# Kernel tuning notes

Measured on AMD Instinct MI355X. Metric: run time of the kernel, lower is better.

Reference implementation:

```python
import jax, jax.numpy as jnp
import numpy as np

B = 65536        # batch of class observations
NUM_CLASSES = 100
D = 128          # embedding_latent_dim / MLP width
H = 64           # rnn_hidden_dim == vq_embedding_dim (must match when use_vq)
K = 512          # vq_num_embeddings
S = 16           # num_splines
A = 6            # spline_action_dim
SQUISH = 0.2
BETA = 0.25      # vq commitment cost


def setup_inputs() -> dict:
    key = jax.random.key(0)
    ks = jax.random.split(key, 32)
    g = lambda i, shape, s=0.05: jax.random.normal(ks[i], shape, jnp.float32) * s
    return dict(
        obs=jax.random.randint(ks[0], (B,), 0, NUM_CLASSES, dtype=jnp.int32),
        embed=g(1, (NUM_CLASSES, D)),
        W1=g(2, (D, D)), b1=jnp.zeros((D,), jnp.float32),
        W2=g(3, (D, D)), b2=jnp.zeros((D,), jnp.float32),
        W3=g(4, (D, D)), b3=jnp.zeros((D,), jnp.float32),
        Wc=g(5, (D, H)), bc=jnp.zeros((H,), jnp.float32),      # carry_init
        Wi=g(6, (D, H)), bi=jnp.zeros((H,), jnp.float32),      # SimpleCell input dense
        Wh=g(7, (H, H)),                                       # SimpleCell recurrent (no bias)
        vq_emb=g(8, (K, H)),                                   # VQ codebook
        Wm=g(9, (H, A)), bm=jnp.zeros((A,), jnp.float32),      # actor mean head
        Ws=g(10, (H, A)), bs=jnp.zeros((A,), jnp.float32),     # actor scale head
        Vw1=g(11, (D, D)), vb1=jnp.zeros((D,), jnp.float32),
        Vw2=g(12, (D, D)), vb2=jnp.zeros((D,), jnp.float32),
        Vw3=g(13, (D, 32)), vb3=jnp.zeros((32,), jnp.float32),
        Vw4=g(14, (32, 1)), vb4=jnp.zeros((1,), jnp.float32),
    )


def reference(obs, embed, W1, b1, W2, b2, W3, b3, Wc, bc, Wi, bi, Wh, vq_emb,
              Wm, bm, Ws, bs, Vw1, vb1, Vw2, vb2, Vw3, vb3, Vw4, vb4):
    # class embedding + ReLU MLP trunk
    z = embed[obs]                                # (B, D)
    z = jax.nn.relu(z @ W1 + b1)
    z = jax.nn.relu(z @ W2 + b2)
    z = jax.nn.relu(z @ W3 + b3)

    carry0 = z @ Wc + bc                          # (B, H) initial RNN carry
    emb_sq = jnp.sum(vq_emb ** 2, axis=1)         # (K,) precomputed codebook norms

    def step(carry, _):
        # SimpleCell: h = tanh(Dense(inputs) + Dense_h(carry)); inputs = z each step
        h = jnp.tanh(z @ Wi + bi + carry @ Wh)    # (B, H)
        # VQ nearest-neighbor lookup
        d = jnp.sum(h ** 2, axis=1, keepdims=True) - 2.0 * (h @ vq_emb.T) + emb_sq  # (B, K)
        idx = jnp.argmin(d, axis=1)               # (B,)
        quant = jnp.take(vq_emb, idx, axis=0)     # (B, H) == one_hot(idx) @ vq_emb
        q = h + jax.lax.stop_gradient(quant - h)  # straight-through estimator
        e_loss = jnp.mean((jax.lax.stop_gradient(q) - h) ** 2)
        q_loss = jnp.mean((q - jax.lax.stop_gradient(h)) ** 2)
        vq_loss_i = q_loss + BETA * e_loss
        # spline heads (use_tanh_last=False -> sigmoid, temp=1)
        am = jax.nn.sigmoid(q @ Wm + bm)                    # (B, A)
        sd = jax.nn.sigmoid(q @ Ws + bs) * SQUISH + 1e-8    # (B, A)
        return q, (am, sd, vq_loss_i, idx)

    _, (ams, sds, losses, idxs) = jax.lax.scan(step, carry0, None, length=S)
    # (S, B, A) -> (B, S*A), matching concatenate along axis 1 in step order
    actor_mean = jnp.transpose(ams, (1, 0, 2)).reshape(B, S * A)
    actor_scale_diag = jnp.transpose(sds, (1, 0, 2)).reshape(B, S * A)

    # critic MLP (tanh activations)
    c = jnp.tanh(z @ Vw1 + vb1)
    c = jnp.tanh(c @ Vw2 + vb2)
    c = jnp.tanh(c @ Vw3 + vb3)
    critic = jnp.squeeze(c @ Vw4 + vb4, axis=-1)  # (B,)

    total_vq_loss = jnp.sum(losses)
    return actor_mean, actor_scale_diag, critic, total_vq_loss, idxs
```

## Files before the change

kernel.cpp:

```cpp
#include <hip/hip_runtime.h>
#include <cmath>


#define D_ 128
#define H_ 64
#define K_ 512
#define S_ 16
#define B_ 65536
#define NTBL_ 64
#define NH_ 16

#define OAM   ((size_t)0)
#define OSD   ((size_t)(B_ * 96))
#define OCRIT ((size_t)(2 * B_ * 96))
#define OLOSS ((size_t)(2 * B_ * 96 + B_))
#define OIDX  ((size_t)(2 * B_ * 96 + B_ + 1))

#define WS_VQWH   0
#define WS_AM8    (512 * 64)
#define WS_SD8    (WS_AM8 + 512 * 8)
#define WS_EMBSQ  (WS_SD8 + 512 * 8)
#define WS_CNTP   (WS_EMBSQ + 512)
#define WS_CLIDX  (WS_CNTP + 2048)
#define WS_CLAM   (WS_CLIDX + 128 * 16)
#define WS_CLSD   (WS_CLAM + 128 * 96)
#define WS_CLCR   (WS_CLSD + 128 * 96)
#define WS_CLLOSS (WS_CLCR + 128)

__device__ int g_tflag = 0;

typedef const __attribute__((address_space(1))) void GASV;
typedef __attribute__((address_space(3))) void LASV;
__device__ __forceinline__ void gll16(const void* g, void* l)
{
    __builtin_amdgcn_global_load_lds((GASV*)g, (LASV*)l, 16, 0, 0);
}

template <int N4>
__device__ __forceinline__ void dma_lin(float4* __restrict__ dst,
                                        const float4* __restrict__ src,
                                        int wid, int lane)
{
    constexpr int PER = N4 / 8;
#pragma unroll
    for (int j = 0; j < PER; j += 64) {
        const int f = wid * PER + j;
        gll16(src + f + lane, dst + f);
    }
}

__global__ __launch_bounds__(512)
__attribute__((amdgpu_waves_per_eu(2, 2)))
void class_kernel(
    const int* __restrict__ obs, int* __restrict__ cnt_part, int nclass,
    const float* __restrict__ embed,
    const float* __restrict__ W1, const float* __restrict__ b1,
    const float* __restrict__ W2, const float* __restrict__ b2,
    const float* __restrict__ W3, const float* __restrict__ b3,
    const float* __restrict__ Wc, const float* __restrict__ bc,
    const float* __restrict__ Wi, const float* __restrict__ bi,
    const float* __restrict__ Wh,
    const float* __restrict__ Wm, const float* __restrict__ bm,
    const float* __restrict__ Wsw, const float* __restrict__ bs,
    const float* __restrict__ Vw1, const float* __restrict__ vb1,
    const float* __restrict__ Vw2, const float* __restrict__ vb2,
    const float* __restrict__ Vw3, const float* __restrict__ vb3,
    const float* __restrict__ Vw4, const float* __restrict__ vb4,
    float* __restrict__ vqwh, float* __restrict__ am8,
    float* __restrict__ sd8, float* __restrict__ embsq,
    const float* __restrict__ vq_emb,
    float* __restrict__ clam, float* __restrict__ clsd,
    float* __restrict__ clcr, float* __restrict__ clidx,
    float* __restrict__ clloss)
{
    extern __shared__ float4 dyn4[];
    float* __restrict__ Af    = reinterpret_cast<float*>(dyn4);
    float* __restrict__ Bf    = reinterpret_cast<float*>(dyn4 + 4096);
    float* __restrict__ vqwhL = reinterpret_cast<float*>(dyn4);
    __shared__ float zA[128], zB[128];
    __shared__ float psum[512];
    __shared__ float t1s[64], c0s[64], c3s[32];
    __shared__ float vw4s[32] __attribute__((aligned(16)));
    __shared__ float Wh_s[64 * 64] __attribute__((aligned(16)));
    __shared__ float hcand[2][4][64] __attribute__((aligned(16)));
    __shared__ float rD2[2][4];
    __shared__ int   rK2[2][4];
    __shared__ int   gk_s[16];
    __shared__ float gd_s[16];
    __shared__ float hh_s[16];

    const int bx   = blockIdx.x;
    const int tid  = threadIdx.x;
    const int lane = tid & 63;
    const int wid  = tid >> 6;

    if (bx < NTBL_) {
        float* __restrict__ er = reinterpret_cast<float*>(dyn4) + wid * 64;
        const int k = bx * 8 + wid;
        er[lane] = vq_emb[k * 64 + lane];
        __syncthreads();

        float acc = 0.f;
#pragma unroll 8
        for (int dd = 0; dd < 64; ++dd)
            acc = fmaf(er[dd], Wh[dd * 64 + lane], acc);
        vqwh[k * 64 + lane] = acc;

        float sq = er[lane] * er[lane];
#pragma unroll
        for (int m = 1; m < 64; m <<= 1) sq += __shfl_xor(sq, m);
        if (lane == 0) embsq[k] = sq;

        if (lane < 8) {
            float vm = 0.f, vs = 0.f;
            if (lane < 6) {
                vm = bm[lane];
                vs = bs[lane];
                for (int dd = 0; dd < 64; ++dd) {
                    vm = fmaf(er[dd], Wm[dd * 6 + lane], vm);
                    vs = fmaf(er[dd], Wsw[dd * 6 + lane], vs);
                }
                vm = 1.f / (1.f + expf(-vm));
                vs = 1.f / (1.f + expf(-vs)) * 0.2f + 1e-8f;
            }
            am8[k * 8 + lane] = vm;
            sd8[k * 8 + lane] = vs;
        }
        __syncthreads();
        if (tid == 0) {
            __threadfence();
            __hip_atomic_fetch_add(&g_tflag, 1, __ATOMIC_RELEASE,
                                   __HIP_MEMORY_SCOPE_AGENT);
        }
        return;
    }

    if (bx < NTBL_ + NH_) {
        int* __restrict__ hsh = reinterpret_cast<int*>(psum);
        if (tid < 128) hsh[tid] = 0;
        __syncthreads();
        const int hb = bx - NTBL_;
        for (int i = hb * 512 + tid; i < B_; i += NH_ * 512)
            atomicAdd(&hsh[obs[i]], 1);
        __syncthreads();
        if (tid < 128) cnt_part[hb * 128 + tid] = hsh[tid];
        return;
    }

    const int c = bx - NTBL_ - NH_;
    const float4* __restrict__ vq4   = reinterpret_cast<const float4*>(vq_emb);
    const float4* __restrict__ vqwh4 = reinterpret_cast<const float4*>(vqwh);

    const int j128 = tid & 127;
    const int q4   = tid >> 7;

    dma_lin<4096>(dyn4, reinterpret_cast<const float4*>(W1), wid, lane);
    if (tid < 128) zA[tid] = embed[c * 128 + tid];
    __syncthreads();

#define DENSE128(SRCW, ZSRC, ZDST, BIAS, ACT)                                  \
    {                                                                          \
        float a0 = 0.f, a1 = 0.f, a2 = 0.f, a3 = 0.f;                          \
        const int i0 = q4 * 32;                                                \
        _Pragma("unroll 8")                                                    \
        for (int ii = 0; ii < 32; ii += 4) {                                   \
            a0 = fmaf(ZSRC[i0 + ii + 0], SRCW[(i0 + ii + 0) * 128 + j128], a0);\
            a1 = fmaf(ZSRC[i0 + ii + 1], SRCW[(i0 + ii + 1) * 128 + j128], a1);\
            a2 = fmaf(ZSRC[i0 + ii + 2], SRCW[(i0 + ii + 2) * 128 + j128], a2);\
            a3 = fmaf(ZSRC[i0 + ii + 3], SRCW[(i0 + ii + 3) * 128 + j128], a3);\
        }                                                                      \
        psum[q4 * 128 + j128] = (a0 + a1) + (a2 + a3);                         \
    }                                                                          \
    __syncthreads();                                                           \
    if (tid < 128) {                                                           \
        float v = BIAS[tid] + ((psum[tid] + psum[128 + tid]) +                 \
                               (psum[256 + tid] + psum[384 + tid]));           \
        ZDST[tid] = ACT;                                                       \
    }                                                                          \
    __syncthreads();

    dma_lin<4096>(dyn4 + 4096, reinterpret_cast<const float4*>(W2), wid, lane);
    DENSE128(Af, zA, zB, b1, fmaxf(v, 0.f))

    dma_lin<4096>(dyn4, reinterpret_cast<const float4*>(W3), wid, lane);
    DENSE128(Bf, zB, zA, b2, fmaxf(v, 0.f))

    dma_lin<2048>(dyn4 + 4096, reinterpret_cast<const float4*>(Wi), wid, lane);
    dma_lin<2048>(dyn4 + 6144, reinterpret_cast<const float4*>(Wc), wid, lane);
    DENSE128(Af, zA, zB, b3, fmaxf(v, 0.f))

    if (tid == 0) {
        while (__hip_atomic_load(&g_tflag, __ATOMIC_RELAXED,
                                 __HIP_MEMORY_SCOPE_AGENT) < NTBL_)
            __builtin_amdgcn_s_sleep(2);
        __builtin_amdgcn_fence(__ATOMIC_ACQUIRE, "agent");
    }
    __syncthreads();

    dma_lin<4096>(dyn4, vqwh4, wid, lane);
    dma_lin<1024>(reinterpret_cast<float4*>(Wh_s),
                  reinterpret_cast<const float4*>(Wh), wid, lane);
    {
        const int jj = tid & 63;
        const int qq = (tid >> 6) & 3;
        const bool isC = tid >= 256;
        const float* __restrict__ Wsrc = isC ? (Bf + 8192) : Bf;
        float a0 = 0.f, a1 = 0.f, a2 = 0.f, a3 = 0.f;
        const int i0 = qq * 32;
#pragma unroll 8
        for (int ii = 0; ii < 32; ii += 4) {
            a0 = fmaf(zB[i0 + ii + 0], Wsrc[(i0 + ii + 0) * 64 + jj], a0);
            a1 = fmaf(zB[i0 + ii + 1], Wsrc[(i0 + ii + 1) * 64 + jj], a1);
            a2 = fmaf(zB[i0 + ii + 2], Wsrc[(i0 + ii + 2) * 64 + jj], a2);
            a3 = fmaf(zB[i0 + ii + 3], Wsrc[(i0 + ii + 3) * 64 + jj], a3);
        }
        psum[(isC ? 256 : 0) + qq * 64 + jj] = (a0 + a1) + (a2 + a3);
    }
    __syncthreads();

    dma_lin<4096>(dyn4 + 4096, vqwh4 + 4096, wid, lane);
    if (tid < 64) {
        t1s[tid] = bi[tid] + ((psum[tid] + psum[64 + tid]) +
                              (psum[128 + tid] + psum[192 + tid]));
    } else if (tid < 128) {
        const int j = tid - 64;
        c0s[j] = bc[j] + ((psum[256 + j] + psum[320 + j]) +
                          (psum[384 + j] + psum[448 + j]));
    } else if (tid < 160) {
        vw4s[tid - 128] = Vw4[tid - 128];
    }
    __syncthreads();

    {
        const int j = lane;
        const int q = wid;
        float a0 = 0.f, a1 = 0.f;
        const int i0 = q * 8;
#pragma unroll
        for (int ii = 0; ii < 8; ii += 2) {
            a0 = fmaf(c0s[i0 + ii + 0], Wh_s[(i0 + ii + 0) * 64 + j], a0);
            a1 = fmaf(c0s[i0 + ii + 1], Wh_s[(i0 + ii + 1) * 64 + j], a1);
        }
        psum[q * 64 + j] = a0 + a1;
    }
    float4 cb[16], cb2[16];
    float esq = 0.f, esq2 = 0.f;
    if (wid < 4) {
        const float4* __restrict__ r1 = vq4 + (size_t)tid * 16;
        const float4* __restrict__ r2 = vq4 + (size_t)(tid + 256) * 16;
#pragma unroll
        for (int d4 = 0; d4 < 16; ++d4) { cb[d4] = r1[d4]; cb2[d4] = r2[d4]; }
#pragma unroll
        for (int d4 = 0; d4 < 16; ++d4) {
            asm volatile("" : "+v"(cb[d4].x), "+v"(cb[d4].y),
                              "+v"(cb[d4].z), "+v"(cb[d4].w));
            asm volatile("" : "+v"(cb2[d4].x), "+v"(cb2[d4].y),
                              "+v"(cb2[d4].z), "+v"(cb2[d4].w));
        }
        esq  = embsq[tid];
        esq2 = embsq[tid + 256];
    }
    __syncthreads();

    if (tid < 64) {
        float a = 0.f;
#pragma unroll
        for (int q = 0; q < 8; ++q) a += psum[q * 64 + tid];
        hcand[0][0][tid] = tanhf(a + t1s[tid]);
    }
    const float t1r = t1s[lane];
    __syncthreads();

    if (wid == 0) {
        const float h0v = hcand[0][0][lane];
        float hh = h0v * h0v;
#pragma unroll
        for (int m = 1; m < 64; m <<= 1) hh += __shfl_xor(hh, m);
        if (lane == 0) hh_s[0] = hh;
    }

    int prevw = 0;
    float ca0 = 0.f, ca1 = 0.f, ca2 = 0.f, ca3 = 0.f;
#pragma unroll 1
    for (int t = 0; t < S_; ++t) {
        const int buf = t & 1;
        if (wid < 4) {
            const float* __restrict__ cur = hcand[buf][prevw];
            float a0 = 0.f, a1 = 0.f, a2 = 0.f, a3 = 0.f;
            float b0 = 0.f, b1_ = 0.f, b2_ = 0.f, b3_ = 0.f;
#pragma unroll
            for (int d4 = 0; d4 < 16; d4 += 4) {
                const float4 h0v = *reinterpret_cast<const float4*>(cur + 4 * d4);
                a0 = fmaf(h0v.x, cb[d4].x, a0); a0 = fmaf(h0v.y, cb[d4].y, a0);
                a0 = fmaf(h0v.z, cb[d4].z, a0); a0 = fmaf(h0v.w, cb[d4].w, a0);
                b0 = fmaf(h0v.x, cb2[d4].x, b0); b0 = fmaf(h0v.y, cb2[d4].y, b0);
                b0 = fmaf(h0v.z, cb2[d4].z, b0); b0 = fmaf(h0v.w, cb2[d4].w, b0);
                const float4 h1v = *reinterpret_cast<const float4*>(cur + 4 * d4 + 4);
                a1 = fmaf(h1v.x, cb[d4 + 1].x, a1); a1 = fmaf(h1v.y, cb[d4 + 1].y, a1);
                a1 = fmaf(h1v.z, cb[d4 + 1].z, a1); a1 = fmaf(h1v.w, cb[d4 + 1].w, a1);
                b1_ = fmaf(h1v.x, cb2[d4 + 1].x, b1_); b1_ = fmaf(h1v.y, cb2[d4 + 1].y, b1_);
                b1_ = fmaf(h1v.z, cb2[d4 + 1].z, b1_); b1_ = fmaf(h1v.w, cb2[d4 + 1].w, b1_);
                const float4 h2v = *reinterpret_cast<const float4*>(cur + 4 * d4 + 8);
                a2 = fmaf(h2v.x, cb[d4 + 2].x, a2); a2 = fmaf(h2v.y, cb[d4 + 2].y, a2);
                a2 = fmaf(h2v.z, cb[d4 + 2].z, a2); a2 = fmaf(h2v.w, cb[d4 + 2].w, a2);
                b2_ = fmaf(h2v.x, cb2[d4 + 2].x, b2_); b2_ = fmaf(h2v.y, cb2[d4 + 2].y, b2_);
                b2_ = fmaf(h2v.z, cb2[d4 + 2].z, b2_); b2_ = fmaf(h2v.w, cb2[d4 + 2].w, b2_);
                const float4 h3v = *reinterpret_cast<const float4*>(cur + 4 * d4 + 12);
                a3 = fmaf(h3v.x, cb[d4 + 3].x, a3); a3 = fmaf(h3v.y, cb[d4 + 3].y, a3);
                a3 = fmaf(h3v.z, cb[d4 + 3].z, a3); a3 = fmaf(h3v.w, cb[d4 + 3].w, a3);
                b3_ = fmaf(h3v.x, cb2[d4 + 3].x, b3_); b3_ = fmaf(h3v.y, cb2[d4 + 3].y, b3_);
                b3_ = fmaf(h3v.z, cb2[d4 + 3].z, b3_); b3_ = fmaf(h3v.w, cb2[d4 + 3].w, b3_);
            }
            const float d1 = fmaf(-2.f, (a0 + a1) + (a2 + a3), esq);
            const float d2 = fmaf(-2.f, (b0 + b1_) + (b2_ + b3_), esq2);
            float bD = d1;
            int   bK = tid;
            if (d2 < bD) { bD = d2; bK = tid + 256; }
#pragma unroll
            for (int m = 1; m < 64; m <<= 1) {
                const float od = __shfl_xor(bD, m);
                const int   ok = __shfl_xor(bK, m);
                if (od < bD || (od == bD && ok < bK)) { bD = od; bK = ok; }
            }
            const float vw = vqwhL[(bK << 6) + lane];
            hcand[buf ^ 1][wid][lane] = tanhf(t1r + vw);
            if (lane == 0) { rD2[buf][wid] = bD; rK2[buf][wid] = bK; }
        } else {
            const int u = tid - 256;
            const int j = u & 127;
            const int hf = u >> 7;
            if (t == 0 || t == 1 || t == 3 || t == 4) {
                const float* __restrict__ W = (t <= 1) ? Vw1 : Vw2;
                const float* __restrict__ zsrc = (t <= 1) ? zB : zA;
                const int i0 = 64 * hf + ((t == 1 || t == 4) ? 32 : 0);
                if (t == 0 || t == 3) { ca0 = ca1 = ca2 = ca3 = 0.f; }
#pragma unroll 8
                for (int ii = 0; ii < 32; ii += 4) {
                    ca0 = fmaf(zsrc[i0 + ii + 0], W[(i0 + ii + 0) * 128 + j], ca0);
                    ca1 = fmaf(zsrc[i0 + ii + 1], W[(i0 + ii + 1) * 128 + j], ca1);
                    ca2 = fmaf(zsrc[i0 + ii + 2], W[(i0 + ii + 2) * 128 + j], ca2);
                    ca3 = fmaf(zsrc[i0 + ii + 3], W[(i0 + ii + 3) * 128 + j], ca3);
                }
                if (t == 1 || t == 4) psum[u] = (ca0 + ca1) + (ca2 + ca3);
            } else if (t == 2) {
                if (u < 128) zA[u] = tanhf(vb1[u] + psum[u] + psum[128 + u]);
            } else if (t == 5) {
                if (u < 128) zA[u] = tanhf(vb2[u] + psum[u] + psum[128 + u]);
            } else if (t == 6) {
                const int j2 = u & 31;
                const int o  = u >> 5;
                float x0 = 0.f, x1 = 0.f;
                const int i0 = 16 * o;
#pragma unroll
                for (int ii = 0; ii < 16; ii += 2) {
                    x0 = fmaf(zA[i0 + ii + 0], Vw3[(i0 + ii + 0) * 32 + j2], x0);
                    x1 = fmaf(zA[i0 + ii + 1], Vw3[(i0 + ii + 1) * 32 + j2], x1);
                }
                psum[u] = x0 + x1;
            } else if (t == 7) {
                if (u < 32) {
                    float v = vb3[u];
#pragma unroll
                    for (int o = 0; o < 8; ++o) v += psum[o * 32 + u];
                    c3s[u] = tanhf(v);
                }
            } else if (t == 8) {
                if (u == 0) {
                    float sm = vb4[0];
#pragma unroll
                    for (int i = 0; i < 32; ++i) sm = fmaf(c3s[i], vw4s[i], sm);
                    clcr[c] = sm;
                }
            }
        }
        __syncthreads();

        float gD = rD2[buf][0];
        int   gK = rK2[buf][0], winw = 0;
#pragma unroll
        for (int w = 1; w < 4; ++w)
            if (rD2[buf][w] < gD || (rD2[buf][w] == gD && rK2[buf][w] < gK)) {
                gD = rD2[buf][w]; gK = rK2[buf][w]; winw = w;
            }
        if (tid == 0) { gk_s[t] = gK; gd_s[t] = gD; }
        prevw = winw;
    }
    __syncthreads();

    for (int tt = wid + 1; tt < S_; tt += 8) {
        const int g = gk_s[tt - 1];
        const float hv = tanhf(t1r + vqwhL[(g << 6) + lane]);
        float hh = hv * hv;
#pragma unroll
        for (int m = 1; m < 64; m <<= 1) hh += __shfl_xor(hh, m);
        if (lane == 0) hh_s[tt] = hh;
    }
    __syncthreads();
    if (tid == 0) {
        float s = 0.f;
#pragma unroll
        for (int t = 0; t < S_; ++t) s += gd_s[t] + hh_s[t];
        clloss[c] = s;
    }

    if (tid < 96) {
        const int t = tid / 6;
        const int j = tid - t * 6;
        const int gk = gk_s[t];
        clam[c * 96 + tid] = am8[gk * 8 + j];
        clsd[c * 96 + tid] = sd8[gk * 8 + j];
    } else if (tid >= 96 && tid < 112) {
        const int t = tid - 96;
        clidx[c * 16 + t] = (float)gk_s[t];
    }
}

__global__ __launch_bounds__(256) void scatter_kernel(
    const int* __restrict__ obs, const float* __restrict__ clam,
    const float* __restrict__ clsd, const float* __restrict__ clcr,
    const float* __restrict__ clidx, const int* __restrict__ cnt_part,
    const float* __restrict__ clloss, int nclass, float* __restrict__ out)
{
    __shared__ int icc_s[128];
    if (blockIdx.x == 0) {
        if (threadIdx.x == 0)
            __hip_atomic_store(&g_tflag, 0, __ATOMIC_RELAXED,
                               __HIP_MEMORY_SCOPE_AGENT);
        if (threadIdx.x < 128) {
            int cc = 0;
#pragma unroll
            for (int p = 0; p < NH_; ++p)
                cc += cnt_part[p * 128 + threadIdx.x];
            icc_s[threadIdx.x] = cc;
        }
        __syncthreads();
        if (threadIdx.x == 0) {
            float s = 0.f;
            for (int c = 0; c < nclass; ++c)
                s += (float)icc_s[c] * clloss[c];
            out[OLOSS] = s * 1.25f / (65536.f * 64.f);
        }
    }

    const int n_am4 = B_ * 24;
    const int n_cr4 = B_ / 4;
    const int n_idx = B_ * 16;
    const int tot   = 2 * n_am4 + n_cr4 + n_idx;
    float4* __restrict__ out4 = reinterpret_cast<float4*>(out);

    for (int i = blockIdx.x * 256 + threadIdx.x; i < tot; i += gridDim.x * 256) {
        if (i < 2 * n_am4) {
            const bool in_am = (i < n_am4);
            const int  i4    = in_am ? i : i - n_am4;
            const uint32_t row =
                (uint32_t)(((uint64_t)(i4 >> 3) * 0xAAAAAAABull) >> 33);
            const int col4 = i4 - (int)row * 24;
            const int cc   = obs[row];
            const float* __restrict__ tab = in_am ? clam : clsd;
            out4[i] = *reinterpret_cast<const float4*>(tab + cc * 96 + col4 * 4);
        } else if (i < 2 * n_am4 + n_cr4) {
            const int j = i - 2 * n_am4;
            const int r = 4 * j;
            float4 v;
            v.x = clcr[obs[r + 0]];
            v.y = clcr[obs[r + 1]];
            v.z = clcr[obs[r + 2]];
            v.w = clcr[obs[r + 3]];
            out4[i] = v;
        } else {
            const int j = i - (2 * n_am4 + n_cr4);
            const int t = j >> 16;
            const int r = j & (B_ - 1);
            out[OIDX + (size_t)j] = clidx[obs[r] * 16 + t];
        }
    }
}

extern "C" void kernel_launch(void* const* d_in, const int* in_sizes, int n_in,
                              void* d_out, int out_size, void* d_ws, size_t ws_size,
                              hipStream_t stream)
{
    const int*   obs   = (const int*)  d_in[0];
    const float* embed = (const float*)d_in[1];
    const float* W1    = (const float*)d_in[2];
    const float* b1    = (const float*)d_in[3];
    const float* W2    = (const float*)d_in[4];
    const float* b2    = (const float*)d_in[5];
    const float* W3    = (const float*)d_in[6];
    const float* b3    = (const float*)d_in[7];
    const float* Wc    = (const float*)d_in[8];
    const float* bc    = (const float*)d_in[9];
    const float* Wi    = (const float*)d_in[10];
    const float* bi    = (const float*)d_in[11];
    const float* Wh    = (const float*)d_in[12];
    const float* vq    = (const float*)d_in[13];
    const float* Wm    = (const float*)d_in[14];
    const float* bm    = (const float*)d_in[15];
    const float* Ws    = (const float*)d_in[16];
    const float* bs    = (const float*)d_in[17];
    const float* Vw1   = (const float*)d_in[18];
    const float* vb1   = (const float*)d_in[19];
    const float* Vw2   = (const float*)d_in[20];
    const float* vb2   = (const float*)d_in[21];
    const float* Vw3   = (const float*)d_in[22];
    const float* vb3   = (const float*)d_in[23];
    const float* Vw4   = (const float*)d_in[24];
    const float* vb4   = (const float*)d_in[25];

    const int nclass = in_sizes[1] / D_;

    float* ws_f     = (float*)d_ws;
    float* vqwh     = ws_f + WS_VQWH;
    float* am8      = ws_f + WS_AM8;
    float* sd8      = ws_f + WS_SD8;
    float* embsq    = ws_f + WS_EMBSQ;
    int*   cnt_part = (int*)(ws_f + WS_CNTP);
    float* clidx    = ws_f + WS_CLIDX;
    float* clam     = ws_f + WS_CLAM;
    float* clsd     = ws_f + WS_CLSD;
    float* clcr     = ws_f + WS_CLCR;
    float* clloss   = ws_f + WS_CLLOSS;

    float* out = (float*)d_out;

    class_kernel<<<NTBL_ + NH_ + nclass, 512, 131072, stream>>>(
        obs, cnt_part, nclass,
        embed, W1, b1, W2, b2, W3, b3, Wc, bc, Wi, bi, Wh,
        Wm, bm, Ws, bs,
        Vw1, vb1, Vw2, vb2, Vw3, vb3, Vw4, vb4,
        vqwh, am8, sd8, embsq, vq,
        clam, clsd, clcr, clidx, clloss);
    scatter_kernel<<<2048, 256, 0, stream>>>(obs, clam, clsd, clcr, clidx,
                                             cnt_part, clloss, nclass, out);
}
```

Before: 59.34 us.

## Move critic MLP layers out of the VQ loop and overlap them with carry setup

The critic's first two dense layers no longer run in pieces inside the first recurrent steps. They now run on the upper four waves at the same time as the lower waves compute the fused carry/input projection and the recurrent product, using a separate partial-sum buffer. The codebook-derived tables move from the workspace to __device__ globals, a few loops are unrolled further, and the acquire fence after the spin-wait on the table flag is removed. That dropped fence risks a memory-ordering bug, and the lower waves now do two recurrent partial products each.

```diff
diff --git a/kernel.cpp b/kernel.cpp
--- a/kernel.cpp
+++ b/kernel.cpp
@@ -16,18 +16,18 @@
 #define OLOSS ((size_t)(2 * B_ * 96 + B_))
 #define OIDX  ((size_t)(2 * B_ * 96 + B_ + 1))
 
-#define WS_VQWH   0
-#define WS_AM8    (512 * 64)
-#define WS_SD8    (WS_AM8 + 512 * 8)
-#define WS_EMBSQ  (WS_SD8 + 512 * 8)
-#define WS_CNTP   (WS_EMBSQ + 512)
-#define WS_CLIDX  (WS_CNTP + 2048)
+#define WS_CLIDX  0
 #define WS_CLAM   (WS_CLIDX + 128 * 16)
 #define WS_CLSD   (WS_CLAM + 128 * 96)
 #define WS_CLCR   (WS_CLSD + 128 * 96)
 #define WS_CLLOSS (WS_CLCR + 128)
 
-__device__ int g_tflag = 0;
+__device__ float g_vqwh[K_ * H_];
+__device__ float g_am8[K_ * 8];
+__device__ float g_sd8[K_ * 8];
+__device__ float g_embsq[K_];
+__device__ int   g_cntp[NH_ * 128];
+__device__ int   g_tflag = 0;
 
 typedef const __attribute__((address_space(1))) void GASV;
 typedef __attribute__((address_space(3))) void LASV;
@@ -52,7 +52,7 @@
 __global__ __launch_bounds__(512)
 __attribute__((amdgpu_waves_per_eu(2, 2)))
 void class_kernel(
-    const int* __restrict__ obs, int* __restrict__ cnt_part, int nclass,
+    const int* __restrict__ obs, int nclass,
     const float* __restrict__ embed,
     const float* __restrict__ W1, const float* __restrict__ b1,
     const float* __restrict__ W2, const float* __restrict__ b2,
@@ -66,8 +66,6 @@
     const float* __restrict__ Vw2, const float* __restrict__ vb2,
     const float* __restrict__ Vw3, const float* __restrict__ vb3,
     const float* __restrict__ Vw4, const float* __restrict__ vb4,
-    float* __restrict__ vqwh, float* __restrict__ am8,
-    float* __restrict__ sd8, float* __restrict__ embsq,
     const float* __restrict__ vq_emb,
     float* __restrict__ clam, float* __restrict__ clsd,
     float* __restrict__ clcr, float* __restrict__ clidx,
@@ -79,6 +77,7 @@
     float* __restrict__ vqwhL = reinterpret_cast<float*>(dyn4);
     __shared__ float zA[128], zB[128];
     __shared__ float psum[512];
+    __shared__ float psumC[256];
     __shared__ float t1s[64], c0s[64], c3s[32];
     __shared__ float vw4s[32] __attribute__((aligned(16)));
     __shared__ float Wh_s[64 * 64] __attribute__((aligned(16)));
@@ -101,21 +100,22 @@
         __syncthreads();
 
         float acc = 0.f;
-#pragma unroll 8
+#pragma unroll 16
         for (int dd = 0; dd < 64; ++dd)
             acc = fmaf(er[dd], Wh[dd * 64 + lane], acc);
-        vqwh[k * 64 + lane] = acc;
+        g_vqwh[k * 64 + lane] = acc;
 
         float sq = er[lane] * er[lane];
 #pragma unroll
         for (int m = 1; m < 64; m <<= 1) sq += __shfl_xor(sq, m);
-        if (lane == 0) embsq[k] = sq;
+        if (lane == 0) g_embsq[k] = sq;
 
         if (lane < 8) {
             float vm = 0.f, vs = 0.f;
             if (lane < 6) {
                 vm = bm[lane];
                 vs = bs[lane];
+#pragma unroll 16
                 for (int dd = 0; dd < 64; ++dd) {
                     vm = fmaf(er[dd], Wm[dd * 6 + lane], vm);
                     vs = fmaf(er[dd], Wsw[dd * 6 + lane], vs);
@@ -123,8 +123,8 @@
                 vm = 1.f / (1.f + expf(-vm));
                 vs = 1.f / (1.f + expf(-vs)) * 0.2f + 1e-8f;
             }
-            am8[k * 8 + lane] = vm;
-            sd8[k * 8 + lane] = vs;
+            g_am8[k * 8 + lane] = vm;
+            g_sd8[k * 8 + lane] = vs;
         }
         __syncthreads();
         if (tid == 0) {
@@ -143,13 +143,14 @@
         for (int i = hb * 512 + tid; i < B_; i += NH_ * 512)
             atomicAdd(&hsh[obs[i]], 1);
         __syncthreads();
-        if (tid < 128) cnt_part[hb * 128 + tid] = hsh[tid];
+        if (tid < 128) g_cntp[hb * 128 + tid] = hsh[tid];
         return;
     }
 
     const int c = bx - NTBL_ - NH_;
     const float4* __restrict__ vq4   = reinterpret_cast<const float4*>(vq_emb);
-    const float4* __restrict__ vqwh4 = reinterpret_cast<const float4*>(vqwh);
+    const float4* __restrict__ vqwh4 =
+        reinterpret_cast<const float4*>(&g_vqwh[0]);
 
     const int j128 = tid & 127;
     const int q4   = tid >> 7;
@@ -193,28 +194,53 @@
         while (__hip_atomic_load(&g_tflag, __ATOMIC_RELAXED,
                                  __HIP_MEMORY_SCOPE_AGENT) < NTBL_)
             __builtin_amdgcn_s_sleep(2);
-        __builtin_amdgcn_fence(__ATOMIC_ACQUIRE, "agent");
     }
     __syncthreads();
 
     dma_lin<4096>(dyn4, vqwh4, wid, lane);
     dma_lin<1024>(reinterpret_cast<float4*>(Wh_s),
                   reinterpret_cast<const float4*>(Wh), wid, lane);
-    {
-        const int jj = tid & 63;
-        const int qq = (tid >> 6) & 3;
-        const bool isC = tid >= 256;
-        const float* __restrict__ Wsrc = isC ? (Bf + 8192) : Bf;
-        float a0 = 0.f, a1 = 0.f, a2 = 0.f, a3 = 0.f;
+    if (wid < 4) {
+        const int jj = lane;
+        const int qq = wid;
         const int i0 = qq * 32;
+        {
+            float a0 = 0.f, a1 = 0.f, a2 = 0.f, a3 = 0.f;
 #pragma unroll 8
-        for (int ii = 0; ii < 32; ii += 4) {
-            a0 = fmaf(zB[i0 + ii + 0], Wsrc[(i0 + ii + 0) * 64 + jj], a0);
-            a1 = fmaf(zB[i0 + ii + 1], Wsrc[(i0 + ii + 1) * 64 + jj], a1);
-            a2 = fmaf(zB[i0 + ii + 2], Wsrc[(i0 + ii + 2) * 64 + jj], a2);
-            a3 = fmaf(zB[i0 + ii + 3], Wsrc[(i0 + ii + 3) * 64 + jj], a3);
-        }
-        psum[(isC ? 256 : 0) + qq * 64 + jj] = (a0 + a1) + (a2 + a3);
+            for (int ii = 0; ii < 32; ii += 4) {
+                a0 = fmaf(zB[i0 + ii + 0], Bf[(i0 + ii + 0) * 64 + jj], a0);
+                a1 = fmaf(zB[i0 + ii + 1], Bf[(i0 + ii + 1) * 64 + jj], a1);
+                a2 = fmaf(zB[i0 + ii + 2], Bf[(i0 + ii + 2) * 64 + jj], a2);
+                a3 = fmaf(zB[i0 + ii + 3], Bf[(i0 + ii + 3) * 64 + jj], a3);
+            }
+            psum[qq * 64 + jj] = (a0 + a1) + (a2 + a3);
+        }
+        {
+            const float* __restrict__ Wsrc = Bf + 8192;
+            float a0 = 0.f, a1 = 0.f, a2 = 0.f, a3 = 0.f;
+#pragma unroll 8
+            for (int ii = 0; ii < 32; ii += 4) {
+                a0 = fmaf(zB[i0 + ii + 0], Wsrc[(i0 + ii + 0) * 64 + jj], a0);
+                a1 = fmaf(zB[i0 + ii + 1], Wsrc[(i0 + ii + 1) * 64 + jj], a1);
+                a2 = fmaf(zB[i0 + ii + 2], Wsrc[(i0 + ii + 2) * 64 + jj], a2);
+                a3 = fmaf(zB[i0 + ii + 3], Wsrc[(i0 + ii + 3) * 64 + jj], a3);
+            }
+            psum[256 + qq * 64 + jj] = (a0 + a1) + (a2 + a3);
+        }
+    } else {
+        const int u = tid - 256;
+        const int j = u & 127;
+        const int hf = u >> 7;
+        const int i0 = 64 * hf;
+        float ca0 = 0.f, ca1 = 0.f, ca2 = 0.f, ca3 = 0.f;
+#pragma unroll 8
+        for (int ii = 0; ii < 64; ii += 4) {
+            ca0 = fmaf(zB[i0 + ii + 0], Vw1[(i0 + ii + 0) * 128 + j], ca0);
+            ca1 = fmaf(zB[i0 + ii + 1], Vw1[(i0 + ii + 1) * 128 + j], ca1);
+            ca2 = fmaf(zB[i0 + ii + 2], Vw1[(i0 + ii + 2) * 128 + j], ca2);
+            ca3 = fmaf(zB[i0 + ii + 3], Vw1[(i0 + ii + 3) * 128 + j], ca3);
+        }
+        psumC[u] = (ca0 + ca1) + (ca2 + ca3);
     }
     __syncthreads();
 
@@ -228,24 +254,28 @@
                           (psum[384 + j] + psum[448 + j]));
     } else if (tid < 160) {
         vw4s[tid - 128] = Vw4[tid - 128];
-    }
-    __syncthreads();
-
-    {
-        const int j = lane;
-        const int q = wid;
-        float a0 = 0.f, a1 = 0.f;
-        const int i0 = q * 8;
-#pragma unroll
-        for (int ii = 0; ii < 8; ii += 2) {
-            a0 = fmaf(c0s[i0 + ii + 0], Wh_s[(i0 + ii + 0) * 64 + j], a0);
-            a1 = fmaf(c0s[i0 + ii + 1], Wh_s[(i0 + ii + 1) * 64 + j], a1);
-        }
-        psum[q * 64 + j] = a0 + a1;
-    }
+    } else if (tid >= 256 && tid < 384) {
+        const int u = tid - 256;
+        zA[u] = tanhf(vb1[u] + psumC[u] + psumC[128 + u]);
+    }
+    __syncthreads();
+
     float4 cb[16], cb2[16];
     float esq = 0.f, esq2 = 0.f;
     if (wid < 4) {
+        const int j = lane;
+#pragma unroll
+        for (int qq2 = 0; qq2 < 2; ++qq2) {
+            const int q = wid + 4 * qq2;
+            float a0 = 0.f, a1 = 0.f;
+            const int i0 = q * 8;
+#pragma unroll
+            for (int ii = 0; ii < 8; ii += 2) {
+                a0 = fmaf(c0s[i0 + ii + 0], Wh_s[(i0 + ii + 0) * 64 + j], a0);
+                a1 = fmaf(c0s[i0 + ii + 1], Wh_s[(i0 + ii + 1) * 64 + j], a1);
+            }
+            psum[q * 64 + j] = a0 + a1;
+        }
         const float4* __restrict__ r1 = vq4 + (size_t)tid * 16;
         const float4* __restrict__ r2 = vq4 + (size_t)(tid + 256) * 16;
 #pragma unroll
@@ -257,8 +287,22 @@
             asm volatile("" : "+v"(cb2[d4].x), "+v"(cb2[d4].y),
                               "+v"(cb2[d4].z), "+v"(cb2[d4].w));
         }
-        esq  = embsq[tid];
-        esq2 = embsq[tid + 256];
+        esq  = g_embsq[tid];
+        esq2 = g_embsq[tid + 256];
+    } else {
+        const int u = tid - 256;
+        const int j = u & 127;
+        const int hf = u >> 7;
+        const int i0 = 64 * hf;
+        float ca0 = 0.f, ca1 = 0.f, ca2 = 0.f, ca3 = 0.f;
+#pragma unroll 8
+        for (int ii = 0; ii < 64; ii += 4) {
+            ca0 = fmaf(zA[i0 + ii + 0], Vw2[(i0 + ii + 0) * 128 + j], ca0);
+            ca1 = fmaf(zA[i0 + ii + 1], Vw2[(i0 + ii + 1) * 128 + j], ca1);
+            ca2 = fmaf(zA[i0 + ii + 2], Vw2[(i0 + ii + 2) * 128 + j], ca2);
+            ca3 = fmaf(zA[i0 + ii + 3], Vw2[(i0 + ii + 3) * 128 + j], ca3);
+        }
+        psumC[u] = (ca0 + ca1) + (ca2 + ca3);
     }
     __syncthreads();
 
@@ -267,6 +311,9 @@
 #pragma unroll
         for (int q = 0; q < 8; ++q) a += psum[q * 64 + tid];
         hcand[0][0][tid] = tanhf(a + t1s[tid]);
+    } else if (tid >= 256 && tid < 384) {
+        const int u = tid - 256;
+        zA[u] = tanhf(vb2[u] + psumC[u] + psumC[128 + u]);
     }
     const float t1r = t1s[lane];
     __syncthreads();
@@ -280,7 +327,6 @@
     }
 
     int prevw = 0;
-    float ca0 = 0.f, ca1 = 0.f, ca2 = 0.f, ca3 = 0.f;
 #pragma unroll 1
     for (int t = 0; t < S_; ++t) {
         const int buf = t & 1;
@@ -327,26 +373,7 @@
             if (lane == 0) { rD2[buf][wid] = bD; rK2[buf][wid] = bK; }
         } else {
             const int u = tid - 256;
-            const int j = u & 127;
-            const int hf = u >> 7;
-            if (t == 0 || t == 1 || t == 3 || t == 4) {
-                const float* __restrict__ W = (t <= 1) ? Vw1 : Vw2;
-                const float* __restrict__ zsrc = (t <= 1) ? zB : zA;
-                const int i0 = 64 * hf + ((t == 1 || t == 4) ? 32 : 0);
-                if (t == 0 || t == 3) { ca0 = ca1 = ca2 = ca3 = 0.f; }
-#pragma unroll 8
-                for (int ii = 0; ii < 32; ii += 4) {
-                    ca0 = fmaf(zsrc[i0 + ii + 0], W[(i0 + ii + 0) * 128 + j], ca0);
-                    ca1 = fmaf(zsrc[i0 + ii + 1], W[(i0 + ii + 1) * 128 + j], ca1);
-                    ca2 = fmaf(zsrc[i0 + ii + 2], W[(i0 + ii + 2) * 128 + j], ca2);
-                    ca3 = fmaf(zsrc[i0 + ii + 3], W[(i0 + ii + 3) * 128 + j], ca3);
-                }
-                if (t == 1 || t == 4) psum[u] = (ca0 + ca1) + (ca2 + ca3);
-            } else if (t == 2) {
-                if (u < 128) zA[u] = tanhf(vb1[u] + psum[u] + psum[128 + u]);
-            } else if (t == 5) {
-                if (u < 128) zA[u] = tanhf(vb2[u] + psum[u] + psum[128 + u]);
-            } else if (t == 6) {
+            if (t == 0) {
                 const int j2 = u & 31;
                 const int o  = u >> 5;
                 float x0 = 0.f, x1 = 0.f;
@@ -356,15 +383,15 @@
                     x0 = fmaf(zA[i0 + ii + 0], Vw3[(i0 + ii + 0) * 32 + j2], x0);
                     x1 = fmaf(zA[i0 + ii + 1], Vw3[(i0 + ii + 1) * 32 + j2], x1);
                 }
-                psum[u] = x0 + x1;
-            } else if (t == 7) {
+                psumC[u] = x0 + x1;
+            } else if (t == 1) {
                 if (u < 32) {
                     float v = vb3[u];
 #pragma unroll
-                    for (int o = 0; o < 8; ++o) v += psum[o * 32 + u];
+                    for (int o = 0; o < 8; ++o) v += psumC[o * 32 + u];
                     c3s[u] = tanhf(v);
                 }
-            } else if (t == 8) {
+            } else if (t == 2) {
                 if (u == 0) {
                     float sm = vb4[0];
 #pragma unroll
@@ -407,8 +434,8 @@
         const int t = tid / 6;
         const int j = tid - t * 6;
         const int gk = gk_s[t];
-        clam[c * 96 + tid] = am8[gk * 8 + j];
-        clsd[c * 96 + tid] = sd8[gk * 8 + j];
+        clam[c * 96 + tid] = g_am8[gk * 8 + j];
+        clsd[c * 96 + tid] = g_sd8[gk * 8 + j];
     } else if (tid >= 96 && tid < 112) {
         const int t = tid - 96;
         clidx[c * 16 + t] = (float)gk_s[t];
@@ -418,7 +445,7 @@
 __global__ __launch_bounds__(256) void scatter_kernel(
     const int* __restrict__ obs, const float* __restrict__ clam,
     const float* __restrict__ clsd, const float* __restrict__ clcr,
-    const float* __restrict__ clidx, const int* __restrict__ cnt_part,
+    const float* __restrict__ clidx,
     const float* __restrict__ clloss, int nclass, float* __restrict__ out)
 {
     __shared__ int icc_s[128];
@@ -430,7 +457,7 @@
             int cc = 0;
 #pragma unroll
             for (int p = 0; p < NH_; ++p)
-                cc += cnt_part[p * 128 + threadIdx.x];
+                cc += g_cntp[p * 128 + threadIdx.x];
             icc_s[threadIdx.x] = cc;
         }
         __syncthreads();
@@ -509,27 +536,22 @@
 
     const int nclass = in_sizes[1] / D_;
 
-    float* ws_f     = (float*)d_ws;
-    float* vqwh     = ws_f + WS_VQWH;
-    float* am8      = ws_f + WS_AM8;
-    float* sd8      = ws_f + WS_SD8;
-    float* embsq    = ws_f + WS_EMBSQ;
-    int*   cnt_part = (int*)(ws_f + WS_CNTP);
-    float* clidx    = ws_f + WS_CLIDX;
-    float* clam     = ws_f + WS_CLAM;
-    float* clsd     = ws_f + WS_CLSD;
-    float* clcr     = ws_f + WS_CLCR;
-    float* clloss   = ws_f + WS_CLLOSS;
+    float* ws_f   = (float*)d_ws;
+    float* clidx  = ws_f + WS_CLIDX;
+    float* clam   = ws_f + WS_CLAM;
+    float* clsd   = ws_f + WS_CLSD;
+    float* clcr   = ws_f + WS_CLCR;
+    float* clloss = ws_f + WS_CLLOSS;
 
     float* out = (float*)d_out;
 
     class_kernel<<<NTBL_ + NH_ + nclass, 512, 131072, stream>>>(
-        obs, cnt_part, nclass,
+        obs, nclass,
         embed, W1, b1, W2, b2, W3, b3, Wc, bc, Wi, bi, Wh,
         Wm, bm, Ws, bs,
         Vw1, vb1, Vw2, vb2, Vw3, vb3, Vw4, vb4,
-        vqwh, am8, sd8, embsq, vq,
+        vq,
         clam, clsd, clcr, clidx, clloss);
     scatter_kernel<<<2048, 256, 0, stream>>>(obs, clam, clsd, clcr, clidx,
-                                             cnt_part, clloss, nclass, out);
+                                             clloss, nclass, out);
 }
```

Measured after the change: 59.66 us. Within noise of the previous version (+0.5%).
